# Kernel optimization log

Measured on AMD Instinct MI355X. Metric: run time of the kernel, lower is better.

## Reference

```python
import jax, jax.numpy as jnp
import numpy as np

N = 8192        # number of particles
NC = 4          # number of cell types (species)
DIM = 3
BOX = 40.0      # box side so typical pair distances straddle the cutoff
EPS_MAX, EPS_MIN = 5.0, 1.0
ALPHA_MAX, ALPHA_MIN = 3.0, 1.0
R_ONSET, R_CUTOFF = 1.7, 2.0


def setup_inputs() -> dict:
    key = jax.random.key(0)
    k_eps, k_alpha, k_ct, k_rad, k_pos = jax.random.split(key, 5)
    epsilon = jax.random.normal(k_eps, (NC, NC), dtype=jnp.float32)
    alpha = jax.random.normal(k_alpha, (NC, NC), dtype=jnp.float32)
    ct_idx = jax.random.randint(k_ct, (N,), 0, NC)
    celltype = jax.nn.one_hot(ct_idx, NC, dtype=jnp.float32)   # [N, NC]
    radius = 0.25 + 0.25 * jax.random.uniform(k_rad, (N, 1), dtype=jnp.float32)
    positions = BOX * jax.random.uniform(k_pos, (N, DIM), dtype=jnp.float32)
    return {"epsilon": epsilon, "alpha": alpha, "celltype": celltype,
            "radius": radius, "positions": positions}


def _species_pairwise(mat, celltype, vmax, vmin):
    # symmetrize as in the original module
    m = 0.5 * (jnp.triu(mat) + jnp.tril(mat).T + jnp.triu(mat).T + jnp.tril(mat))
    m = m - jnp.eye(NC, dtype=mat.dtype) * 0.5 * jnp.diagonal(m)
    m = jax.nn.sigmoid(m) * vmax + vmin
    m = celltype @ m @ celltype.T                               # [N, N]
    alive = celltype.sum(-1) > 0.0                              # [N] -> masks columns
    return jnp.where(alive, m, 0.0)


def reference(epsilon, alpha, celltype, radius, positions):
    eps_m = _species_pairwise(epsilon, celltype, EPS_MAX, EPS_MIN)    # [N, N]
    alpha_m = _species_pairwise(alpha, celltype, ALPHA_MAX, ALPHA_MIN)
    sigma_m = radius + radius.T                                       # [N, N]

    diff = positions[:, None, :] - positions[None, :, :]              # [N, N, 3]
    dr2 = jnp.sum(diff * diff, axis=-1)                               # [N, N]
    eye = jnp.eye(N, dtype=bool)
    dr = jnp.sqrt(jnp.where(eye, 1.0, dr2))                           # safe sqrt on diag

    # Morse potential (jax_md.energy.morse)
    u = eps_m * jnp.square(1.0 - jnp.exp(-alpha_m * (dr - sigma_m))) - eps_m

    # multiplicative isotropic cutoff (jax_md smoothing, operates on r^2)
    r_o, r_c = R_ONSET ** 2, R_CUTOFF ** 2
    smooth_inner = jnp.square(r_c - dr2) * (r_c + 2.0 * dr2 - 3.0 * r_o) / (r_c - r_o) ** 3
    smooth = jnp.where(dr2 < r_o, 1.0, jnp.where(dr2 < r_c, smooth_inner, 0.0))

    e = jnp.where(eye, 0.0, u * smooth)                               # mask self-interaction
    return 0.5 * jnp.sum(e)                                           # scalar total energy
```

## Files before the change

kernel.cpp:

```cpp
#include <hip/hip_runtime.h>
#include <hip/hip_bf16.h>

#define NPART 8192
#define NCT 4
#define TPB 256

__device__ __forceinline__ float loadf(const void* p, int idx, bool bf) {
    if (bf) {
        unsigned int u = ((const unsigned short*)p)[idx];
        return __uint_as_float(u << 16);
    }
    return ((const float*)p)[idx];
}

__global__ void zero_kernel(float* acc) { *acc = 0.0f; }

__global__ __launch_bounds__(TPB) void pair_kernel(const void* __restrict__ eps,
                                                   const void* __restrict__ alp,
                                                   const void* __restrict__ ct,
                                                   const void* __restrict__ rad,
                                                   const void* __restrict__ pos,
                                                   float* __restrict__ acc_out)
{
    __shared__ float4 sp[TPB];
    __shared__ int ssp[TPB];
    __shared__ float stab[32];
    __shared__ float red[TPB / 64];

    const int t = threadIdx.x;

    unsigned int w = ((const unsigned int*)ct)[t & 63];
    const bool bf = (__ballot((w & 0xFFFFu) != 0) != 0ull);

    if (t < 16) {
        int a = t >> 2, b = t & 3;
        float me = (a == b) ? loadf(eps, a * NCT + a, bf)
                            : 0.5f * (loadf(eps, a * NCT + b, bf) + loadf(eps, b * NCT + a, bf));
        float ma = (a == b) ? loadf(alp, a * NCT + a, bf)
                            : 0.5f * (loadf(alp, a * NCT + b, bf) + loadf(alp, b * NCT + a, bf));
        stab[t]      = 5.0f / (1.0f + __expf(-me)) + 1.0f;
        stab[16 + t] = 3.0f / (1.0f + __expf(-ma)) + 1.0f;
    }

    const int j0 = blockIdx.y * TPB;
    {
        int j = j0 + t;
        float4 pj;
        pj.x = loadf(pos, j * 3 + 0, bf);
        pj.y = loadf(pos, j * 3 + 1, bf);
        pj.z = loadf(pos, j * 3 + 2, bf);
        pj.w = loadf(rad, j, bf);
        sp[t] = pj;
        int sj = -1;
#pragma unroll
        for (int c = 0; c < NCT; ++c)
            if (loadf(ct, j * NCT + c, bf) > 0.5f) sj = c;
        ssp[t] = sj;
    }

    const int i = blockIdx.x * TPB + t;
    float4 pi;
    pi.x = loadf(pos, i * 3 + 0, bf);
    pi.y = loadf(pos, i * 3 + 1, bf);
    pi.z = loadf(pos, i * 3 + 2, bf);
    pi.w = loadf(rad, i, bf);
    int si = -1;
#pragma unroll
    for (int c = 0; c < NCT; ++c)
        if (loadf(ct, i * NCT + c, bf) > 0.5f) si = c;

    __syncthreads();

    constexpr float RC2 = 4.0f;
    constexpr float RO2 = 1.7f * 1.7f;
    constexpr float C1  = RC2 - 3.0f * RO2;
    const float INV_D = 1.0f / ((RC2 - RO2) * (RC2 - RO2) * (RC2 - RO2));

    float acc = 0.0f;
    if (si >= 0) {
#pragma unroll 4
        for (int jj = 0; jj < TPB; ++jj) {
            float4 pj = sp[jj];
            float dx = pi.x - pj.x;
            float dy = pi.y - pj.y;
            float dz = pi.z - pj.z;
            float dr2 = fmaf(dx, dx, fmaf(dy, dy, dz * dz));
            if (dr2 < RC2) {
                int j = j0 + jj;
                int sj = ssp[jj];
                if (j != i && sj >= 0) {
                    float e = stab[(si << 2) | sj];
                    float a = stab[16 + ((si << 2) | sj)];
                    float dr = sqrtf(dr2);
                    float ex = __expf(-a * (dr - (pi.w + pj.w)));
                    float om = 1.0f - ex;
                    float u = fmaf(e * om, om, -e);
                    float smooth = 1.0f;
                    if (dr2 >= RO2) {
                        float d = RC2 - dr2;
                        smooth = d * d * fmaf(2.0f, dr2, C1) * INV_D;
                    }
                    acc += u * smooth;
                }
            }
        }
    }

#pragma unroll
    for (int off = 32; off > 0; off >>= 1) acc += __shfl_down(acc, off, 64);
    int lane = t & 63, wv = t >> 6;
    if (lane == 0) red[wv] = acc;
    __syncthreads();
    if (t == 0) {
        float s = red[0] + red[1] + red[2] + red[3];
        atomicAdd(acc_out, 0.5f * s);
    }
}

__global__ void finalize_kernel(const float* __restrict__ acc,
                                const void* __restrict__ ct,
                                void* __restrict__ out)
{
    bool bf = false;
    const unsigned int* cw = (const unsigned int*)ct;
    for (int k = 0; k < 64; ++k) bf |= (cw[k] & 0xFFFFu) != 0;
    float v = acc[0];
    if (bf) ((__hip_bfloat16*)out)[0] = __float2bfloat16(v);
    else    ((float*)out)[0] = v;
}

extern "C" void kernel_launch(void* const* d_in, const int* in_sizes, int n_in,
                              void* d_out, int out_size, void* d_ws, size_t ws_size,
                              hipStream_t stream)
{
    const void* eps = nullptr; const void* alp = nullptr;
    const void* ct = nullptr;  const void* rad = nullptr; const void* pos = nullptr;
    int nsmall = 0;
    for (int k = 0; k < n_in; ++k) {
        int s = in_sizes[k];
        if (s == NCT * NCT)        { if (nsmall++ == 0) eps = d_in[k]; else alp = d_in[k]; }
        else if (s == NPART * NCT) ct  = d_in[k];
        else if (s == NPART)       rad = d_in[k];
        else if (s == NPART * 3)   pos = d_in[k];
    }
    if (!eps || !alp || !ct || !rad || !pos) {
        eps = d_in[0]; alp = d_in[1]; ct = d_in[2]; rad = d_in[3]; pos = d_in[4];
    }

    float* acc = (float*)d_ws;

    zero_kernel<<<1, 1, 0, stream>>>(acc);
    dim3 grid(NPART / TPB, NPART / TPB);
    pair_kernel<<<grid, TPB, 0, stream>>>(eps, alp, ct, rad, pos, acc);
    finalize_kernel<<<1, 1, 0, stream>>>(acc, ct, d_out);
}
```

Before: 96.85 us.

## Exploit pair symmetry with triangular tile grid and deterministic partial reduction

Launches only upper-triangular tile pairs (528 instead of 1024 blocks), mapping the linear block index to (bx, by) and halving the contribution of diagonal tiles. Off-diagonal tiles count each pair once and are no longer scaled by 0.5. This relies on the energy being symmetric in i and j. The atomic accumulation and the zero kernel are replaced by per-block partials summed in a parallel finalize kernel, and the inner loop unroll rises from 4 to 8. The partials buffer is 528 floats and must fit in the workspace.

Measured after the change: 90.00 us. 1.08x faster.

```diff
diff --git a/kernel.cpp b/kernel.cpp
--- a/kernel.cpp
+++ b/kernel.cpp
@@ -4,6 +4,8 @@
 #define NPART 8192
 #define NCT 4
 #define TPB 256
+#define NTILE (NPART / TPB)
+#define NBLK (NTILE * (NTILE + 1) / 2)
 
 __device__ __forceinline__ float loadf(const void* p, int idx, bool bf) {
     if (bf) {
@@ -13,14 +15,12 @@
     return ((const float*)p)[idx];
 }
 
-__global__ void zero_kernel(float* acc) { *acc = 0.0f; }
-
 __global__ __launch_bounds__(TPB) void pair_kernel(const void* __restrict__ eps,
                                                    const void* __restrict__ alp,
                                                    const void* __restrict__ ct,
                                                    const void* __restrict__ rad,
                                                    const void* __restrict__ pos,
-                                                   float* __restrict__ acc_out)
+                                                   float* __restrict__ partials)
 {
     __shared__ float4 sp[TPB];
     __shared__ int ssp[TPB];
@@ -32,17 +32,24 @@
     unsigned int w = ((const unsigned int*)ct)[t & 63];
     const bool bf = (__ballot((w & 0xFFFFu) != 0) != 0ull);
 
+    const int b = blockIdx.x;
+    int by = (int)((sqrtf(8.0f * (float)b + 1.0f) - 1.0f) * 0.5f);
+    while ((by + 1) * (by + 2) / 2 <= b) ++by;
+    while (by * (by + 1) / 2 > b) --by;
+    const int bx = b - by * (by + 1) / 2;
+    const bool diag = (bx == by);
+
     if (t < 16) {
-        int a = t >> 2, b = t & 3;
-        float me = (a == b) ? loadf(eps, a * NCT + a, bf)
-                            : 0.5f * (loadf(eps, a * NCT + b, bf) + loadf(eps, b * NCT + a, bf));
-        float ma = (a == b) ? loadf(alp, a * NCT + a, bf)
-                            : 0.5f * (loadf(alp, a * NCT + b, bf) + loadf(alp, b * NCT + a, bf));
+        int a = t >> 2, c = t & 3;
+        float me = (a == c) ? loadf(eps, a * NCT + a, bf)
+                            : 0.5f * (loadf(eps, a * NCT + c, bf) + loadf(eps, c * NCT + a, bf));
+        float ma = (a == c) ? loadf(alp, a * NCT + a, bf)
+                            : 0.5f * (loadf(alp, a * NCT + c, bf) + loadf(alp, c * NCT + a, bf));
         stab[t]      = 5.0f / (1.0f + __expf(-me)) + 1.0f;
         stab[16 + t] = 3.0f / (1.0f + __expf(-ma)) + 1.0f;
     }
 
-    const int j0 = blockIdx.y * TPB;
+    const int j0 = by * TPB;
     {
         int j = j0 + t;
         float4 pj;
@@ -58,7 +65,7 @@
         ssp[t] = sj;
     }
 
-    const int i = blockIdx.x * TPB + t;
+    const int i = bx * TPB + t;
     float4 pi;
     pi.x = loadf(pos, i * 3 + 0, bf);
     pi.y = loadf(pos, i * 3 + 1, bf);
@@ -78,7 +85,7 @@
 
     float acc = 0.0f;
     if (si >= 0) {
-#pragma unroll 4
+#pragma unroll 8
         for (int jj = 0; jj < TPB; ++jj) {
             float4 pj = sp[jj];
             float dx = pi.x - pj.x;
@@ -106,27 +113,38 @@
         }
     }
 
+    acc *= diag ? 0.5f : 1.0f;
+
 #pragma unroll
     for (int off = 32; off > 0; off >>= 1) acc += __shfl_down(acc, off, 64);
     int lane = t & 63, wv = t >> 6;
     if (lane == 0) red[wv] = acc;
     __syncthreads();
-    if (t == 0) {
-        float s = red[0] + red[1] + red[2] + red[3];
-        atomicAdd(acc_out, 0.5f * s);
-    }
+    if (t == 0) partials[b] = red[0] + red[1] + red[2] + red[3];
 }
 
-__global__ void finalize_kernel(const float* __restrict__ acc,
-                                const void* __restrict__ ct,
-                                void* __restrict__ out)
+__global__ __launch_bounds__(TPB) void finalize_kernel(const float* __restrict__ partials,
+                                                       const void* __restrict__ ct,
+                                                       void* __restrict__ out)
 {
-    bool bf = false;
-    const unsigned int* cw = (const unsigned int*)ct;
-    for (int k = 0; k < 64; ++k) bf |= (cw[k] & 0xFFFFu) != 0;
-    float v = acc[0];
-    if (bf) ((__hip_bfloat16*)out)[0] = __float2bfloat16(v);
-    else    ((float*)out)[0] = v;
+    __shared__ float red[TPB / 64];
+    const int t = threadIdx.x;
+
+    unsigned int w = ((const unsigned int*)ct)[t & 63];
+    const bool bf = (__ballot((w & 0xFFFFu) != 0) != 0ull);
+
+    float s = 0.0f;
+    for (int k = t; k < NBLK; k += TPB) s += partials[k];
+#pragma unroll
+    for (int off = 32; off > 0; off >>= 1) s += __shfl_down(s, off, 64);
+    int lane = t & 63, wv = t >> 6;
+    if (lane == 0) red[wv] = s;
+    __syncthreads();
+    if (t == 0) {
+        float v = red[0] + red[1] + red[2] + red[3];
+        if (bf) ((__hip_bfloat16*)out)[0] = __float2bfloat16(v);
+        else    ((float*)out)[0] = v;
+    }
 }
 
 extern "C" void kernel_launch(void* const* d_in, const int* in_sizes, int n_in,
@@ -147,10 +165,8 @@
         eps = d_in[0]; alp = d_in[1]; ct = d_in[2]; rad = d_in[3]; pos = d_in[4];
     }
 
-    float* acc = (float*)d_ws;
+    float* partials = (float*)d_ws;
 
-    zero_kernel<<<1, 1, 0, stream>>>(acc);
-    dim3 grid(NPART / TPB, NPART / TPB);
-    pair_kernel<<<grid, TPB, 0, stream>>>(eps, alp, ct, rad, pos, acc);
-    finalize_kernel<<<1, 1, 0, stream>>>(acc, ct, d_out);
+    pair_kernel<<<NBLK, TPB, 0, stream>>>(eps, alp, ct, rad, pos, partials);
+    finalize_kernel<<<1, TPB, 0, stream>>>(partials, ct, d_out);
 }
```
